# Kernel optimization log

Measured on AMD Instinct MI355X. Metric: run time of the kernel, lower is better.

The kernel has to match this reference:

```python
import jax, jax.numpy as jnp
import numpy as np

B, T, DIM, H = 2, 2048, 1024, 16
HD = DIM // H  # head_dim = 64
ROPE_BASE = 10000.0


def setup_inputs() -> dict:
    key = jax.random.key(0)
    k1, k2, k3, k4 = jax.random.split(key, 4)
    s = 1.0 / np.sqrt(DIM)
    return {
        "x": jax.random.normal(k1, (B, T, DIM), dtype=jnp.float32),
        "Wqkv": jax.random.normal(k2, (DIM, 3 * DIM), dtype=jnp.float32) * s,
        "Wout": jax.random.normal(k3, (DIM, DIM), dtype=jnp.float32) * s,
        "bout": jax.random.normal(k4, (DIM,), dtype=jnp.float32) * 0.01,
    }


def _rotate_half(x):
    # interleaved rotation: (x0,x1,x2,x3,...) -> (-x1,x0,-x3,x2,...)
    x1 = x[..., ::2]
    x2 = x[..., 1::2]
    return jnp.stack((-x2, x1), axis=-1).reshape(x.shape)


def _rope_cos_sin(seq_len, dtype):
    inv_freq = 1.0 / (ROPE_BASE ** (jnp.arange(0, HD, 2, dtype=jnp.float32) / HD))
    t = jnp.arange(seq_len, dtype=jnp.float32)
    freqs = t[:, None] * inv_freq[None, :]          # [T, HD/2]
    emb = jnp.concatenate((freqs, freqs), axis=-1)  # [T, HD] (cat layout, as in source)
    return jnp.cos(emb).astype(dtype), jnp.sin(emb).astype(dtype)


def reference(x, Wqkv, Wout, bout):
    b, t, _ = x.shape
    qkv = x @ Wqkv                                  # [B, T, 3*DIM]
    q, k, v = jnp.split(qkv, 3, axis=-1)
    # b t (h d) -> b h t d
    reshape = lambda z: z.reshape(b, t, H, HD).transpose(0, 2, 1, 3)
    q, k, v = reshape(q), reshape(k), reshape(v)
    cos, sin = _rope_cos_sin(t, x.dtype)            # [T, HD]
    q = q * cos + _rotate_half(q) * sin
    k = k * cos + _rotate_half(k) * sin
    scale = HD ** -0.5
    scores = jnp.einsum("bhqd,bhkd->bhqk", q, k) * scale
    attn = jax.nn.softmax(scores, axis=-1)
    out = jnp.einsum("bhqk,bhkd->bhqd", attn, v)    # [B, H, T, HD]
    out = out.transpose(0, 2, 1, 3).reshape(b, t, DIM)
    return out @ Wout + bout
```

## Files before the change

### kernel.cpp

```cpp
#include <hip/hip_runtime.h>
#include <math.h>


typedef unsigned short u16;
typedef __attribute__((ext_vector_type(8))) short short8;
typedef __attribute__((ext_vector_type(4))) short short4v;
typedef __attribute__((ext_vector_type(4))) float f32x4;
typedef __attribute__((ext_vector_type(16))) float f32x16;

#define T_SEQ 2048

#if __has_builtin(__builtin_amdgcn_exp2f)
#define EXP2(x) __builtin_amdgcn_exp2f(x)
#else
#define EXP2(x) exp2f(x)
#endif

__device__ __forceinline__ float b2f(u16 u) {
    union { unsigned int i; float f; } x; x.i = ((unsigned int)u) << 16; return x.f;
}
__device__ __forceinline__ u16 f2b(float f) {
    union { float f; unsigned int i; } x; x.f = f;
    return (u16)((x.i + 0x7FFFu + ((x.i >> 16) & 1u)) >> 16);
}
__device__ __forceinline__ void gl_lds16(const u16* g, u16* l) {
    __builtin_amdgcn_global_load_lds(
        (const __attribute__((address_space(1))) unsigned int*)g,
        (__attribute__((address_space(3))) unsigned int*)l, 16, 0, 0);
}
__device__ __forceinline__ short4v pack4(float a, float b, float c, float d) {
    union { float f; unsigned int u; } xa, xb, xc, xd;
    xa.f = a; xb.f = b; xc.f = c; xd.f = d;
    union { unsigned int u2[2]; short4v s; } r;
    r.u2[0] = (xa.u >> 16) | (xb.u & 0xffff0000u);
    r.u2[1] = (xc.u >> 16) | (xd.u & 0xffff0000u);
    return r.s;
}

__global__ __launch_bounds__(256) void setup_kernel(
    const float* __restrict__ x, const float* __restrict__ Wqkv,
    const float* __restrict__ Wout, u16* __restrict__ xb,
    u16* __restrict__ WqkvT, u16* __restrict__ WoutT,
    float* __restrict__ costab, float* __restrict__ sintab)
{
    const int bid = blockIdx.x;
    const int tid = threadIdx.x;

    if (bid < 4096) {
        int i = (bid * 256 + tid) * 4;
        float4 v = *(const float4*)(x + i);
        ushort4 w;
        w.x = f2b(v.x); w.y = f2b(v.y); w.z = f2b(v.z); w.w = f2b(v.w);
        *(ushort4*)(xb + i) = w;
        return;
    }
    if (bid < 8192) {
        const float* in; u16* out; int R, Cn, bx, by;
        if (bid < 7168) { in = Wqkv; out = WqkvT; R = 1024; Cn = 3072;
                          int id = bid - 4096; bx = id % 96; by = id / 96; }
        else            { in = Wout; out = WoutT; R = 1024; Cn = 1024;
                          int id = bid - 7168; bx = id & 31; by = id >> 5; }
        __shared__ u16 tile[32][33];
        const int tx = tid & 31, ty = tid >> 5;
        const int r0 = by * 32, c0 = bx * 32;
#pragma unroll
        for (int rr = ty; rr < 32; rr += 8)
            tile[tx][rr] = f2b(in[(size_t)(r0 + rr) * Cn + c0 + tx]);
        __syncthreads();
#pragma unroll
        for (int rr = ty; rr < 32; rr += 8)
            out[(size_t)(c0 + rr) * R + r0 + tx] = tile[rr][tx];
        return;
    }
    {
        int idx = (bid - 8192) * 256 + tid;
        int t = idx >> 6, d = idx & 63;
        const float nl32 = -0.28782313662425576f;
        float f = __expf((float)(d & 31) * nl32);
        float s, c;
        __sincosf((float)t * f, &s, &c);
        costab[idx] = c; sintab[idx] = s;
    }
}

template<int OBF>
__global__ __launch_bounds__(256) void gemm_bt_mfma(
    const u16* __restrict__ A, const u16* __restrict__ Bt,
    void* __restrict__ Cv, const float* __restrict__ bias,
    int M, int N, int K)
{
    __shared__ u16 As[128 * 32];
    __shared__ u16 Bs[128 * 32];

    const int tid = threadIdx.x;
    const int wave = tid >> 6, lane = tid & 63;
    const int col = lane & 15, quad = lane >> 4;
    const int wm = (wave & 1) * 64, wn = (wave >> 1) * 64;
    const int m0 = blockIdx.y * 128, n0 = blockIdx.x * 128;

    f32x4 acc[4][4];
#pragma unroll
    for (int i = 0; i < 4; ++i)
#pragma unroll
        for (int j = 0; j < 4; ++j) acc[i][j] = f32x4{0.f, 0.f, 0.f, 0.f};

    const int c1 = tid, c2 = tid + 256;
    const u16* a1 = A + (size_t)(m0 + (c1 >> 2)) * K + (c1 & 3) * 8;
    const u16* a2 = A + (size_t)(m0 + (c2 >> 2)) * K + (c2 & 3) * 8;
    const u16* b1 = Bt + (size_t)(n0 + (c1 >> 2)) * K + (c1 & 3) * 8;
    const u16* b2 = Bt + (size_t)(n0 + (c2 >> 2)) * K + (c2 & 3) * 8;
    u16* la1 = As + c1 * 8; u16* la2 = As + c2 * 8;
    u16* lb1 = Bs + c1 * 8; u16* lb2 = Bs + c2 * 8;

    for (int k0 = 0; k0 < K; k0 += 32) {
        __syncthreads();
        gl_lds16(a1 + k0, la1);
        gl_lds16(a2 + k0, la2);
        gl_lds16(b1 + k0, lb1);
        gl_lds16(b2 + k0, lb2);
        __syncthreads();

        short8 af[4], bfr[4];
#pragma unroll
        for (int i = 0; i < 4; ++i) {
            af[i]  = *(const short8*)&As[(wm + i * 16 + col) * 32 + quad * 8];
            bfr[i] = *(const short8*)&Bs[(wn + i * 16 + col) * 32 + quad * 8];
        }
#pragma unroll
        for (int i = 0; i < 4; ++i)
#pragma unroll
            for (int j = 0; j < 4; ++j)
                acc[i][j] = __builtin_amdgcn_mfma_f32_16x16x32_bf16(
                    af[i], bfr[j], acc[i][j], 0, 0, 0);
    }

#pragma unroll
    for (int j = 0; j < 4; ++j) {
        int n = n0 + wn + j * 16 + col;
        float bv = bias ? bias[n] : 0.f;
#pragma unroll
        for (int i = 0; i < 4; ++i) {
            int mbase = m0 + wm + i * 16 + quad * 4;
#pragma unroll
            for (int r = 0; r < 4; ++r) {
                if (OBF) ((u16*)Cv)[(size_t)(mbase + r) * N + n] = f2b(acc[i][j][r] + bv);
                else     ((float*)Cv)[(size_t)(mbase + r) * N + n] = acc[i][j][r] + bv;
            }
        }
    }
}

__global__ __launch_bounds__(256) void prep_kernel(
    const u16* __restrict__ qkvb, const float* __restrict__ costab,
    const float* __restrict__ sintab, u16* __restrict__ Qb,
    u16* __restrict__ Kb, u16* __restrict__ Vimg)
{
    __shared__ u16 Vls[64][72];

    const int tid = threadIdx.x;
    const int bh = blockIdx.y;
    const int t0 = blockIdx.x * 64;
    const int b = bh >> 4, h = bh & 15;
    const int t_loc = tid >> 2;
    const int d0 = (tid & 3) * 16;

    const int t = t0 + t_loc;
    const u16* qp = qkvb + ((size_t)(b * T_SEQ + t)) * 3072 + h * 64 + d0;

    float ct[16], st[16];
    {
        const float* cp = costab + (size_t)t * 64 + d0;
        const float* sp = sintab + (size_t)t * 64 + d0;
#pragma unroll
        for (int j = 0; j < 16; j += 4) {
            *(float4*)&ct[j] = *(const float4*)(cp + j);
            *(float4*)&st[j] = *(const float4*)(sp + j);
        }
    }

#pragma unroll
    for (int part = 0; part < 2; ++part) {
        const float sc = part ? 1.f : 0.18033688011112042f;
        const u16* src = qp + part * 1024;
        u16* dst = (part ? Kb : Qb) + ((size_t)(bh * T_SEQ + t)) * 64 + d0;
        short8 v0 = *(const short8*)(src);
        short8 v1 = *(const short8*)(src + 8);
        float f[16];
#pragma unroll
        for (int j = 0; j < 8; ++j) { f[j] = b2f((u16)v0[j]); f[8 + j] = b2f((u16)v1[j]); }
        u16 o[16];
#pragma unroll
        for (int i = 0; i < 8; ++i) {
            float e = f[2 * i], od = f[2 * i + 1];
            o[2 * i]     = f2b((e * ct[2 * i]      - od * st[2 * i]) * sc);
            o[2 * i + 1] = f2b((od * ct[2 * i + 1] + e  * st[2 * i + 1]) * sc);
        }
        *(short8*)(dst)     = *(short8*)&o[0];
        *(short8*)(dst + 8) = *(short8*)&o[8];
    }

    {
        const u16* src = qp + 2048;
        *(short8*)&Vls[t_loc][d0]     = *(const short8*)(src);
        *(short8*)&Vls[t_loc][d0 + 8] = *(const short8*)(src + 8);
    }
    __syncthreads();
    {
        const int dt    = tid >> 7;
        const int g     = (tid >> 5) & 3;
        const int hi2   = (tid >> 4) & 1;
        const int dpair = tid & 15;
        const int kl0 = g * 8 + hi2 * 4;
        const int d0v = dt * 32 + 2 * dpair;
        const int kt_base = blockIdx.x * 2;
#pragma unroll
        for (int ktl = 0; ktl < 2; ++ktl) {
            u16 o[8];
#pragma unroll
            for (int j = 0; j < 4; ++j) {
                o[j]     = Vls[ktl * 32 + kl0 + j][d0v];
                o[4 + j] = Vls[ktl * 32 + kl0 + j][d0v + 1];
            }
            u16* dst = Vimg + ((size_t)(bh * 64 + kt_base + ktl)) * 2048 + tid * 8;
            *(short8*)dst = *(short8*)&o[0];
        }
    }
}

__global__ __launch_bounds__(256, 3) void attn32_kernel(
    const u16* __restrict__ Qb, const u16* __restrict__ Kb,
    const u16* __restrict__ Vimg, float* __restrict__ po, float* __restrict__ pl)
{
    __shared__ u16 Kbuf[2][2][2048];
    __shared__ u16 Vbuf[2][2][2048];

    const int tid = threadIdx.x;
    const int wave = tid >> 6, lane = tid & 63;
    const int qcol = lane & 31;
    const int hi = lane >> 5;

    const int bid = blockIdx.x;
    const int bh = bid >> 5;
    const int seg = (bid >> 4) & 1;
    const int qblk = bid & 15;
    const int qrow0 = qblk * 128 + wave * 32;

    short8 qa[4];
    {
        const u16* qp = Qb + ((size_t)(bh * T_SEQ + qrow0 + qcol)) * 64 + hi * 8;
#pragma unroll
        for (int c = 0; c < 4; ++c) qa[c] = *(const short8*)(qp + c * 16);
    }

    f32x16 O0, O1;
#pragma unroll
    for (int i = 0; i < 16; ++i) { O0[i] = 0.f; O1[i] = 0.f; }
    float Lacc = 0.f;

    const u16* kg_ptr = Kb + ((size_t)bh * T_SEQ + qcol) * 64 + wave * 16 + hi * 8;
    const u16* vg_ptr = Vimg + ((size_t)bh * 64) * 2048 + tid * 8;

    const int kt0 = seg * 32;

    gl_lds16(kg_ptr + (size_t)kt0 * 2048,       &Kbuf[0][0][tid * 8]);
    gl_lds16(kg_ptr + (size_t)(kt0 + 1) * 2048, &Kbuf[0][1][tid * 8]);
    gl_lds16(vg_ptr + (size_t)kt0 * 2048,       &Vbuf[0][0][tid * 8]);
    gl_lds16(vg_ptr + (size_t)(kt0 + 1) * 2048, &Vbuf[0][1][tid * 8]);
    __syncthreads();

    for (int r = 0; r < 16; ++r) {
        const int cur = r & 1;

        short8 kf[2][4];
        short4v vv[2][8];
#pragma unroll
        for (int half = 0; half < 2; ++half) {
#pragma unroll
            for (int f = 0; f < 4; ++f)
                kf[half][f] = *(const short8*)&Kbuf[cur][half][(f * 64 + lane) * 8];
#pragma unroll
            for (int g = 0; g < 4; ++g) {
                vv[half][2 * g]     = *(const short4v*)&Vbuf[cur][half][g * 256 + lane * 4];
                vv[half][2 * g + 1] = *(const short4v*)&Vbuf[cur][half][1024 + g * 256 + lane * 4];
            }
        }

        if (r < 15) {
            const int kt = kt0 + (r + 1) * 2;
            gl_lds16(kg_ptr + (size_t)kt * 2048,       &Kbuf[cur ^ 1][0][tid * 8]);
            gl_lds16(kg_ptr + (size_t)(kt + 1) * 2048, &Kbuf[cur ^ 1][1][tid * 8]);
            gl_lds16(vg_ptr + (size_t)kt * 2048,       &Vbuf[cur ^ 1][0][tid * 8]);
            gl_lds16(vg_ptr + (size_t)(kt + 1) * 2048, &Vbuf[cur ^ 1][1][tid * 8]);
        }

#pragma unroll
        for (int half = 0; half < 2; ++half) {
            f32x16 sT;
#pragma unroll
            for (int ii = 0; ii < 16; ++ii) sT[ii] = 0.f;
#pragma unroll
            for (int c = 0; c < 4; ++c)
                sT = __builtin_amdgcn_mfma_f32_32x32x16_bf16(kf[half][c], qa[c], sT, 0, 0, 0);

            float pe[16];
#pragma unroll
            for (int ii = 0; ii < 16; ++ii) pe[ii] = EXP2(sT[ii]);
            short4v pb[4];
#pragma unroll
            for (int g = 0; g < 4; ++g) {
                pb[g] = pack4(pe[4 * g + 0], pe[4 * g + 1],
                              pe[4 * g + 2], pe[4 * g + 3]);
                Lacc += (pe[4 * g + 0] + pe[4 * g + 1]) +
                        (pe[4 * g + 2] + pe[4 * g + 3]);
            }

#pragma unroll
            for (int g = 0; g < 4; ++g) {
                O0 = __builtin_amdgcn_mfma_f32_32x32x8bf16_1k(vv[half][2 * g],     pb[g], O0, 0, 0, 0);
                O1 = __builtin_amdgcn_mfma_f32_32x32x8bf16_1k(vv[half][2 * g + 1], pb[g], O1, 0, 0, 0);
            }
        }

        __syncthreads();
    }

    float Lq = Lacc + __shfl(Lacc, lane ^ 32);

    const size_t prow = ((size_t)(seg * 32 + bh)) * T_SEQ + qrow0 + qcol;
    float* op = po + prow * 64;
#pragma unroll
    for (int g2 = 0; g2 < 4; ++g2) {
        int dd = g2 * 8 + hi * 4;
        *(float4*)(op + dd)      = make_float4(O0[4 * g2 + 0], O0[4 * g2 + 1],
                                               O0[4 * g2 + 2], O0[4 * g2 + 3]);
        *(float4*)(op + 32 + dd) = make_float4(O1[4 * g2 + 0], O1[4 * g2 + 1],
                                               O1[4 * g2 + 2], O1[4 * g2 + 3]);
    }
    if (hi == 0) pl[prow] = Lq;
}

__global__ __launch_bounds__(256) void attn_combine_kernel(
    const float* __restrict__ po, const float* __restrict__ pl,
    u16* __restrict__ aob)
{
    const int idx = blockIdx.x * 256 + (int)threadIdx.x;
    const int row = idx >> 4;
    const int d4 = idx & 15;

    float4 o0 = *(const float4*)(po + (size_t)row * 64 + d4 * 4);
    float4 o1 = *(const float4*)(po + ((size_t)row + 65536) * 64 + d4 * 4);
    float L = pl[row] + pl[row + 65536];
    float inv = 1.f / L;

    const int bh = row >> 11, t = row & 2047;
    const int b = bh >> 4, h = bh & 15;
    ushort4 w;
    w.x = f2b((o0.x + o1.x) * inv);
    w.y = f2b((o0.y + o1.y) * inv);
    w.z = f2b((o0.z + o1.z) * inv);
    w.w = f2b((o0.w + o1.w) * inv);
    *(ushort4*)(aob + ((size_t)(b * T_SEQ + t)) * 1024 + h * 64 + d4 * 4) = w;
}

extern "C" void kernel_launch(void* const* d_in, const int* in_sizes, int n_in,
                              void* d_out, int out_size, void* d_ws, size_t ws_size,
                              hipStream_t stream)
{
    const float* x    = (const float*)d_in[0];
    const float* Wqkv = (const float*)d_in[1];
    const float* Wout = (const float*)d_in[2];
    const float* bout = (const float*)d_in[3];
    float* out = (float*)d_out;

    char* w = (char*)d_ws;
    u16* qkvb    = (u16*)(w);
    u16* xb      = (u16*)(w + 25165824);
    u16* WqkvT   = (u16*)(w + 33554432);
    u16* WoutT   = (u16*)(w + 39845888);
    u16* aob     = (u16*)(w + 41943040);
    u16* Qb      = (u16*)(w + 50331648);
    u16* Kb      = (u16*)(w + 58720256);
    u16* Vimg    = (u16*)(w + 67108864);
    float* ctab  = (float*)(w + 75497472);
    float* stab  = (float*)(w + 76021760);
    float* po    = (float*)(w);
    float* pl    = (float*)(w + 33554432);

    dim3 blk(256);
    setup_kernel<<<dim3(8704), blk, 0, stream>>>(x, Wqkv, Wout, xb, WqkvT, WoutT, ctab, stab);
    gemm_bt_mfma<1><<<dim3(24, 32), blk, 0, stream>>>(xb, WqkvT, qkvb, nullptr, 4096, 3072, 1024);
    prep_kernel<<<dim3(32, 32), blk, 0, stream>>>(qkvb, ctab, stab, Qb, Kb, Vimg);
    attn32_kernel<<<dim3(1024), blk, 0, stream>>>(Qb, Kb, Vimg, po, pl);
    attn_combine_kernel<<<dim3(4096), blk, 0, stream>>>(po, pl, aob);
    gemm_bt_mfma<0><<<dim3(8, 32), blk, 0, stream>>>(aob, WoutT, out, bout, 4096, 1024, 1024);
}
```

Before: 214.2 us.

## Process two 32-row query tiles per wave to reuse K/V fragments

Each wave now handles 64 query rows (two 32-row sub-tiles) instead of 32, so every K/V tile staged in LDS and loaded into registers feeds twice the MFMA work. The grid is halved to 512 blocks and the block index is remapped so neighbouring blocks land on different heads and segments. Occupancy is lowered from 3 to 2 blocks per SM to make room for the doubled accumulators and Q fragments. The cost is heavier register pressure and fewer blocks to spread across the CUs.

```diff
diff --git a/kernel.cpp b/kernel.cpp
--- a/kernel.cpp
+++ b/kernel.cpp
@@ -227,7 +227,7 @@
     }
 }
 
-__global__ __launch_bounds__(256, 3) void attn32_kernel(
+__global__ __launch_bounds__(256, 2) void attn32_kernel(
     const u16* __restrict__ Qb, const u16* __restrict__ Kb,
     const u16* __restrict__ Vimg, float* __restrict__ po, float* __restrict__ pl)
 {
@@ -240,22 +240,24 @@
     const int hi = lane >> 5;
 
     const int bid = blockIdx.x;
-    const int bh = bid >> 5;
-    const int seg = (bid >> 4) & 1;
-    const int qblk = bid & 15;
-    const int qrow0 = qblk * 128 + wave * 32;
-
-    short8 qa[4];
-    {
-        const u16* qp = Qb + ((size_t)(bh * T_SEQ + qrow0 + qcol)) * 64 + hi * 8;
-#pragma unroll
-        for (int c = 0; c < 4; ++c) qa[c] = *(const short8*)(qp + c * 16);
-    }
-
-    f32x16 O0, O1;
-#pragma unroll
-    for (int i = 0; i < 16; ++i) { O0[i] = 0.f; O1[i] = 0.f; }
-    float Lacc = 0.f;
+    const int lbid = (bid & 7) * 64 + (bid >> 3);
+    const int bh = lbid >> 4;
+    const int seg = (lbid >> 3) & 1;
+    const int qblk = lbid & 7;
+    const int qrow0 = qblk * 256 + wave * 64;
+
+    short8 qa[2][4];
+#pragma unroll
+    for (int qs = 0; qs < 2; ++qs) {
+        const u16* qp = Qb + ((size_t)(bh * T_SEQ + qrow0 + qs * 32 + qcol)) * 64 + hi * 8;
+#pragma unroll
+        for (int c = 0; c < 4; ++c) qa[qs][c] = *(const short8*)(qp + c * 16);
+    }
+
+    f32x16 O00, O01, O10, O11;
+#pragma unroll
+    for (int i = 0; i < 16; ++i) { O00[i] = 0.f; O01[i] = 0.f; O10[i] = 0.f; O11[i] = 0.f; }
+    float Lacc0 = 0.f, Lacc1 = 0.f;
 
     const u16* kg_ptr = Kb + ((size_t)bh * T_SEQ + qcol) * 64 + wave * 16 + hi * 8;
     const u16* vg_ptr = Vimg + ((size_t)bh * 64) * 2048 + tid * 8;
@@ -295,48 +297,76 @@
 
 #pragma unroll
         for (int half = 0; half < 2; ++half) {
-            f32x16 sT;
-#pragma unroll
-            for (int ii = 0; ii < 16; ++ii) sT[ii] = 0.f;
-#pragma unroll
-            for (int c = 0; c < 4; ++c)
-                sT = __builtin_amdgcn_mfma_f32_32x32x16_bf16(kf[half][c], qa[c], sT, 0, 0, 0);
-
-            float pe[16];
-#pragma unroll
-            for (int ii = 0; ii < 16; ++ii) pe[ii] = EXP2(sT[ii]);
-            short4v pb[4];
-#pragma unroll
-            for (int g = 0; g < 4; ++g) {
-                pb[g] = pack4(pe[4 * g + 0], pe[4 * g + 1],
-                              pe[4 * g + 2], pe[4 * g + 3]);
-                Lacc += (pe[4 * g + 0] + pe[4 * g + 1]) +
-                        (pe[4 * g + 2] + pe[4 * g + 3]);
-            }
-
-#pragma unroll
-            for (int g = 0; g < 4; ++g) {
-                O0 = __builtin_amdgcn_mfma_f32_32x32x8bf16_1k(vv[half][2 * g],     pb[g], O0, 0, 0, 0);
-                O1 = __builtin_amdgcn_mfma_f32_32x32x8bf16_1k(vv[half][2 * g + 1], pb[g], O1, 0, 0, 0);
+            f32x16 sT0, sT1;
+#pragma unroll
+            for (int ii = 0; ii < 16; ++ii) { sT0[ii] = 0.f; sT1[ii] = 0.f; }
+#pragma unroll
+            for (int c = 0; c < 4; ++c) {
+                sT0 = __builtin_amdgcn_mfma_f32_32x32x16_bf16(kf[half][c], qa[0][c], sT0, 0, 0, 0);
+                sT1 = __builtin_amdgcn_mfma_f32_32x32x16_bf16(kf[half][c], qa[1][c], sT1, 0, 0, 0);
+            }
+
+            {
+                float pe[16];
+#pragma unroll
+                for (int ii = 0; ii < 16; ++ii) pe[ii] = EXP2(sT0[ii]);
+                short4v pb[4];
+#pragma unroll
+                for (int g = 0; g < 4; ++g) {
+                    pb[g] = pack4(pe[4 * g + 0], pe[4 * g + 1],
+                                  pe[4 * g + 2], pe[4 * g + 3]);
+                    Lacc0 += (pe[4 * g + 0] + pe[4 * g + 1]) +
+                             (pe[4 * g + 2] + pe[4 * g + 3]);
+                }
+#pragma unroll
+                for (int g = 0; g < 4; ++g) {
+                    O00 = __builtin_amdgcn_mfma_f32_32x32x8bf16_1k(vv[half][2 * g],     pb[g], O00, 0, 0, 0);
+                    O01 = __builtin_amdgcn_mfma_f32_32x32x8bf16_1k(vv[half][2 * g + 1], pb[g], O01, 0, 0, 0);
+                }
+            }
+            {
+                float pe[16];
+#pragma unroll
+                for (int ii = 0; ii < 16; ++ii) pe[ii] = EXP2(sT1[ii]);
+                short4v pb[4];
+#pragma unroll
+                for (int g = 0; g < 4; ++g) {
+                    pb[g] = pack4(pe[4 * g + 0], pe[4 * g + 1],
+                                  pe[4 * g + 2], pe[4 * g + 3]);
+                    Lacc1 += (pe[4 * g + 0] + pe[4 * g + 1]) +
+                             (pe[4 * g + 2] + pe[4 * g + 3]);
+                }
+#pragma unroll
+                for (int g = 0; g < 4; ++g) {
+                    O10 = __builtin_amdgcn_mfma_f32_32x32x8bf16_1k(vv[half][2 * g],     pb[g], O10, 0, 0, 0);
+                    O11 = __builtin_amdgcn_mfma_f32_32x32x8bf16_1k(vv[half][2 * g + 1], pb[g], O11, 0, 0, 0);
+                }
             }
         }
 
         __syncthreads();
     }
 
-    float Lq = Lacc + __shfl(Lacc, lane ^ 32);
-
-    const size_t prow = ((size_t)(seg * 32 + bh)) * T_SEQ + qrow0 + qcol;
-    float* op = po + prow * 64;
+    float Lq0 = Lacc0 + __shfl(Lacc0, lane ^ 32);
+    float Lq1 = Lacc1 + __shfl(Lacc1, lane ^ 32);
+
+    const size_t prow0 = ((size_t)(seg * 32 + bh)) * T_SEQ + qrow0 + qcol;
+    const size_t prow1 = prow0 + 32;
+    float* op0 = po + prow0 * 64;
+    float* op1 = po + prow1 * 64;
 #pragma unroll
     for (int g2 = 0; g2 < 4; ++g2) {
         int dd = g2 * 8 + hi * 4;
-        *(float4*)(op + dd)      = make_float4(O0[4 * g2 + 0], O0[4 * g2 + 1],
-                                               O0[4 * g2 + 2], O0[4 * g2 + 3]);
-        *(float4*)(op + 32 + dd) = make_float4(O1[4 * g2 + 0], O1[4 * g2 + 1],
-                                               O1[4 * g2 + 2], O1[4 * g2 + 3]);
-    }
-    if (hi == 0) pl[prow] = Lq;
+        *(float4*)(op0 + dd)      = make_float4(O00[4 * g2 + 0], O00[4 * g2 + 1],
+                                                O00[4 * g2 + 2], O00[4 * g2 + 3]);
+        *(float4*)(op0 + 32 + dd) = make_float4(O01[4 * g2 + 0], O01[4 * g2 + 1],
+                                                O01[4 * g2 + 2], O01[4 * g2 + 3]);
+        *(float4*)(op1 + dd)      = make_float4(O10[4 * g2 + 0], O10[4 * g2 + 1],
+                                                O10[4 * g2 + 2], O10[4 * g2 + 3]);
+        *(float4*)(op1 + 32 + dd) = make_float4(O11[4 * g2 + 0], O11[4 * g2 + 1],
+                                                O11[4 * g2 + 2], O11[4 * g2 + 3]);
+    }
+    if (hi == 0) { pl[prow0] = Lq0; pl[prow1] = Lq1; }
 }
 
 __global__ __launch_bounds__(256) void attn_combine_kernel(
@@ -390,7 +420,7 @@
     setup_kernel<<<dim3(8704), blk, 0, stream>>>(x, Wqkv, Wout, xb, WqkvT, WoutT, ctab, stab);
     gemm_bt_mfma<1><<<dim3(24, 32), blk, 0, stream>>>(xb, WqkvT, qkvb, nullptr, 4096, 3072, 1024);
     prep_kernel<<<dim3(32, 32), blk, 0, stream>>>(qkvb, ctab, stab, Qb, Kb, Vimg);
-    attn32_kernel<<<dim3(1024), blk, 0, stream>>>(Qb, Kb, Vimg, po, pl);
+    attn32_kernel<<<dim3(512), blk, 0, stream>>>(Qb, Kb, Vimg, po, pl);
     attn_combine_kernel<<<dim3(4096), blk, 0, stream>>>(po, pl, aob);
     gemm_bt_mfma<0><<<dim3(8, 32), blk, 0, stream>>>(aob, WoutT, out, bout, 4096, 1024, 1024);
 }
```

After: 211.7 us. About the same (-1.2%).
